# Kernel tuning notes

Hardware: AMD Instinct MI355X
Metric: run time of the kernel (lower is better)

## Reference

```python
import jax, jax.numpy as jnp
import numpy as np

B, S, E, D_ENT, D_HID, D_ATT = 8, 512, 32, 256, 512, 200

def setup_inputs() -> dict:
    key = jax.random.key(0)
    k1, k2, k3, k4, k5 = jax.random.split(key, 5)
    return {
        "cxt": jax.random.normal(k1, (B, S, D_HID), dtype=jnp.float32),
        "ent": jax.random.normal(k2, (B, S, E, D_ENT), dtype=jnp.float32),
        "We": jax.random.normal(k3, (D_ENT, D_ATT), dtype=jnp.float32) * 0.05,
        "Wh": jax.random.normal(k4, (D_HID, D_ATT), dtype=jnp.float32) * 0.05,
        "Ws": jax.random.normal(k5, (D_ATT, 1), dtype=jnp.float32) * 0.05,
    }

def reference(cxt, ent, We, Wh, Ws):
    # cxt: [B,S,H], ent: [B,S,E,D]
    cmean = jnp.mean(cxt, axis=1)                      # [B,H]  (mean context)
    h_att = cmean @ Wh                                 # [B,A]  shared across (s,e)
    e_att = jnp.einsum('bsed,da->bsea', ent, We)       # [B,S,E,A]
    M = jnp.tanh(h_att[:, None, None, :] + e_att)      # [B,S,E,A]
    S_logits = jnp.einsum('bsea,ao->bse', M, Ws)       # [B,S,E] (Ws has out dim 1)
    S_att = jax.nn.softmax(S_logits, axis=-1)          # softmax over entities
    # diag-matmul + sum in the original == weighted sum over entities
    ent_att = jnp.einsum('bse,bsed->bsd', S_att, ent)  # [B,S,D]
    return ent_att
```

## Files before the change

### kernel.cpp

```cpp
#include <hip/hip_runtime.h>
#include <math.h>

#define NB 8
#define NS 512
#define NE 32
#define DE 256
#define DH 512
#define DA 200
#define DAP 224
#define NJ 7

typedef __bf16 bf16x8 __attribute__((ext_vector_type(8)));
typedef float f32x16 __attribute__((ext_vector_type(16)));

__device__ __forceinline__ float tanh_fast(float x) {
    float e = __expf(x + x);
    return fmaf(-2.f, __builtin_amdgcn_rcpf(e + 1.f), 1.f);
}

__global__ __launch_bounds__(256) void cmean_partial(const float* __restrict__ cxt,
                                                     float* __restrict__ psum) {
    const int g = blockIdx.x;
    const int b = g >> 6, c = g & 63;
    const int t = threadIdx.x;
    const float* base = cxt + ((size_t)b * NS + c * 8) * DH;
    float s0 = 0.f, s1 = 0.f;
    #pragma unroll
    for (int s = 0; s < 8; ++s) {
        s0 += base[s * DH + t];
        s1 += base[s * DH + t + 256];
    }
    psum[(size_t)g * DH + t]       = s0;
    psum[(size_t)g * DH + t + 256] = s1;
}

__global__ __launch_bounds__(256) void hatt_from_psum(const float* __restrict__ psum,
                                                      const float* __restrict__ Wh,
                                                      float* __restrict__ hattw) {
    const int b = blockIdx.x;
    const int t = threadIdx.x;
    __shared__ float cm[DH];
    float s0 = 0.f, s1 = 0.f;
    for (int c = 0; c < 64; ++c) {
        s0 += psum[((size_t)b * 64 + c) * DH + t];
        s1 += psum[((size_t)b * 64 + c) * DH + t + 256];
    }
    cm[t]       = s0 * (1.f / NS);
    cm[t + 256] = s1 * (1.f / NS);
    __syncthreads();
    if (t < DAP) {
        float acc = 0.f;
        if (t < DA)
            for (int h = 0; h < DH; ++h)
                acc = fmaf(cm[h], Wh[h * DA + t], acc);
        hattw[b * DAP + t] = acc;
    }
}

__global__ __launch_bounds__(64) void wef_build(const float* __restrict__ We,
                                                __bf16* __restrict__ wef) {
    const int f = blockIdx.x;
    const int l = threadIdx.x;
    const int nj = f >> 4, kk = f & 15;
    const int n = nj * 32 + (l & 31);
    bf16x8 v;
    #pragma unroll
    for (int e = 0; e < 8; ++e) {
        int K = kk * 16 + ((l >> 5) << 2) + (e & 3) + 8 * (e >> 2);
        v[e] = (__bf16)((n < DA) ? We[K * DA + n] : 0.f);
    }
    reinterpret_cast<bf16x8*>(wef)[f * 64 + l] = v;
}

__global__ __launch_bounds__(1024) void entatt_main(const float* __restrict__ ent,
                                                    const __bf16* __restrict__ wef,
                                                    const float* __restrict__ hattw,
                                                    const float* __restrict__ Ws,
                                                    float* __restrict__ out) {
    const int t    = threadIdx.x;
    const int lane = t & 63;
    const int wid  = t >> 6;
    const int g    = blockIdx.x;
    const int bs   = g * 16 + wid;
    const int b    = g >> 5;

    __shared__ __bf16 wef_lds[NJ * 16 * 512];
    __shared__ float  hatt_lds[DAP];
    __shared__ float  ws_lds[DAP];
    __shared__ float  lg_lds[16][NE];

    {
        const float4* s4 = reinterpret_cast<const float4*>(wef);
        float4* d4 = reinterpret_cast<float4*>(wef_lds);
        #pragma unroll
        for (int i = 0; i < NJ; ++i) d4[t + i * 1024] = s4[t + i * 1024];
    }
    if (t < DAP) {
        hatt_lds[t] = hattw[b * DAP + t];
        ws_lds[t]   = (t < DA) ? Ws[t] : 0.f;
    }

    __syncthreads();

    const int m  = lane & 31;
    const int hi = lane >> 5;
    const float* eb = ent + (size_t)bs * (NE * DE);

    bf16x8 A[16];
    #pragma unroll
    for (int kk = 0; kk < 16; ++kk) {
        const float* p = eb + m * DE + kk * 16 + hi * 4;
        float4 u0 = *reinterpret_cast<const float4*>(p);
        float4 u1 = *reinterpret_cast<const float4*>(p + 8);
        bf16x8 v = { (__bf16)u0.x, (__bf16)u0.y, (__bf16)u0.z, (__bf16)u0.w,
                     (__bf16)u1.x, (__bf16)u1.y, (__bf16)u1.z, (__bf16)u1.w };
        A[kk] = v;
    }

    const bf16x8* w8 = reinterpret_cast<const bf16x8*>(wef_lds);

    float part[16];
    #pragma unroll
    for (int r = 0; r < 16; ++r) part[r] = 0.f;

    #pragma unroll 1
    for (int nj = 0; nj < NJ; ++nj) {
        f32x16 acc;
        #pragma unroll
        for (int r = 0; r < 16; ++r) acc[r] = 0.f;
        #pragma unroll
        for (int kk = 0; kk < 16; ++kk)
            acc = __builtin_amdgcn_mfma_f32_32x32x16_bf16(
                      A[kk], w8[(nj * 16 + kk) * 64 + lane], acc, 0, 0, 0);
        const float ha  = hatt_lds[nj * 32 + m];
        const float wsa = ws_lds[nj * 32 + m];
        #pragma unroll
        for (int r = 0; r < 16; ++r)
            part[r] = fmaf(tanh_fast(acc[r] + ha), wsa, part[r]);
    }

    #pragma unroll
    for (int r = 0; r < 16; ++r) {
        float v = part[r];
        v += __shfl_xor(v, 1);  v += __shfl_xor(v, 2);  v += __shfl_xor(v, 4);
        v += __shfl_xor(v, 8);  v += __shfl_xor(v, 16);
        part[r] = v;
    }
    if (m == 0) {
        #pragma unroll
        for (int r = 0; r < 16; ++r)
            lg_lds[wid][(r & 3) + 8 * (r >> 2) + 4 * hi] = part[r];
    }

    float mx = -1e30f;
    #pragma unroll
    for (int e = 0; e < NE; ++e) mx = fmaxf(mx, lg_lds[wid][e]);

    const float4* eb4 = reinterpret_cast<const float4*>(eb);
    float wsum = 0.f;
    float4 o = make_float4(0.f, 0.f, 0.f, 0.f);
    #pragma unroll
    for (int e = 0; e < NE; ++e) {
        float w = __expf(lg_lds[wid][e] - mx);
        wsum += w;
        float4 v = eb4[e * 64 + lane];
        o.x = fmaf(w, v.x, o.x); o.y = fmaf(w, v.y, o.y);
        o.z = fmaf(w, v.z, o.z); o.w = fmaf(w, v.w, o.w);
    }
    const float inv = __builtin_amdgcn_rcpf(wsum);
    float4 res = make_float4(o.x * inv, o.y * inv, o.z * inv, o.w * inv);
    reinterpret_cast<float4*>(out)[(size_t)bs * 64 + lane] = res;
}

extern "C" void kernel_launch(void* const* d_in, const int* in_sizes, int n_in,
                              void* d_out, int out_size, void* d_ws, size_t ws_size,
                              hipStream_t stream) {
    const float* cxt = (const float*)d_in[0];
    const float* ent = (const float*)d_in[1];
    const float* We  = (const float*)d_in[2];
    const float* Wh  = (const float*)d_in[3];
    const float* Ws  = (const float*)d_in[4];
    float* out = (float*)d_out;

    float*  psum  = (float*)d_ws;
    float*  hattw = psum + 512 * DH;
    __bf16* wef   = (__bf16*)(hattw + NB * DAP);

    hipLaunchKernelGGL(wef_build, dim3(NJ * 16), dim3(64), 0, stream, We, wef);
    hipLaunchKernelGGL(cmean_partial, dim3(512), dim3(256), 0, stream, cxt, psum);
    hipLaunchKernelGGL(hatt_from_psum, dim3(NB), dim3(256), 0, stream, psum, Wh, hattw);
    hipLaunchKernelGGL(entatt_main, dim3(256), dim3(1024), 0, stream,
                       ent, wef, hattw, Ws, out);
}
```

Measured before the change: 78.51 us.

## Process two (b,s) rows per wave with prefetch of second tile during compute

```diff
diff --git a/kernel.cpp b/kernel.cpp
--- a/kernel.cpp
+++ b/kernel.cpp
@@ -72,51 +72,16 @@
     reinterpret_cast<bf16x8*>(wef)[f * 64 + l] = v;
 }
 
-__global__ __launch_bounds__(1024) void entatt_main(const float* __restrict__ ent,
-                                                    const __bf16* __restrict__ wef,
-                                                    const float* __restrict__ hattw,
-                                                    const float* __restrict__ Ws,
-                                                    float* __restrict__ out) {
-    const int t    = threadIdx.x;
-    const int lane = t & 63;
-    const int wid  = t >> 6;
-    const int g    = blockIdx.x;
-    const int bs   = g * 16 + wid;
-    const int b    = g >> 5;
-
-    __shared__ __bf16 wef_lds[NJ * 16 * 512];
-    __shared__ float  hatt_lds[DAP];
-    __shared__ float  ws_lds[DAP];
-    __shared__ float  lg_lds[16][NE];
-
-    {
-        const float4* s4 = reinterpret_cast<const float4*>(wef);
-        float4* d4 = reinterpret_cast<float4*>(wef_lds);
-        #pragma unroll
-        for (int i = 0; i < NJ; ++i) d4[t + i * 1024] = s4[t + i * 1024];
-    }
-    if (t < DAP) {
-        hatt_lds[t] = hattw[b * DAP + t];
-        ws_lds[t]   = (t < DA) ? Ws[t] : 0.f;
-    }
-
-    __syncthreads();
-
+__device__ __forceinline__ void compute_tile(const bf16x8 (&A)[16],
+                                             const __bf16* __restrict__ wef_lds,
+                                             const float* __restrict__ hatt_lds,
+                                             const float* __restrict__ ws_lds,
+                                             const float* __restrict__ eb,
+                                             float* __restrict__ out,
+                                             float* __restrict__ lg_scratch,
+                                             int bs, int lane) {
     const int m  = lane & 31;
     const int hi = lane >> 5;
-    const float* eb = ent + (size_t)bs * (NE * DE);
-
-    bf16x8 A[16];
-    #pragma unroll
-    for (int kk = 0; kk < 16; ++kk) {
-        const float* p = eb + m * DE + kk * 16 + hi * 4;
-        float4 u0 = *reinterpret_cast<const float4*>(p);
-        float4 u1 = *reinterpret_cast<const float4*>(p + 8);
-        bf16x8 v = { (__bf16)u0.x, (__bf16)u0.y, (__bf16)u0.z, (__bf16)u0.w,
-                     (__bf16)u1.x, (__bf16)u1.y, (__bf16)u1.z, (__bf16)u1.w };
-        A[kk] = v;
-    }
-
     const bf16x8* w8 = reinterpret_cast<const bf16x8*>(wef_lds);
 
     float part[16];
@@ -149,19 +114,19 @@
     if (m == 0) {
         #pragma unroll
         for (int r = 0; r < 16; ++r)
-            lg_lds[wid][(r & 3) + 8 * (r >> 2) + 4 * hi] = part[r];
+            lg_scratch[(r & 3) + 8 * (r >> 2) + 4 * hi] = part[r];
     }
 
     float mx = -1e30f;
     #pragma unroll
-    for (int e = 0; e < NE; ++e) mx = fmaxf(mx, lg_lds[wid][e]);
+    for (int e = 0; e < NE; ++e) mx = fmaxf(mx, lg_scratch[e]);
 
     const float4* eb4 = reinterpret_cast<const float4*>(eb);
     float wsum = 0.f;
     float4 o = make_float4(0.f, 0.f, 0.f, 0.f);
     #pragma unroll
     for (int e = 0; e < NE; ++e) {
-        float w = __expf(lg_lds[wid][e] - mx);
+        float w = __expf(lg_scratch[e] - mx);
         wsum += w;
         float4 v = eb4[e * 64 + lane];
         o.x = fmaf(w, v.x, o.x); o.y = fmaf(w, v.y, o.y);
@@ -170,6 +135,83 @@
     const float inv = __builtin_amdgcn_rcpf(wsum);
     float4 res = make_float4(o.x * inv, o.y * inv, o.z * inv, o.w * inv);
     reinterpret_cast<float4*>(out)[(size_t)bs * 64 + lane] = res;
+}
+
+__global__ __launch_bounds__(512) void entatt_main(const float* __restrict__ ent,
+                                                   const __bf16* __restrict__ wef,
+                                                   const float* __restrict__ hattw,
+                                                   const float* __restrict__ Ws,
+                                                   float* __restrict__ out) {
+    const int t    = threadIdx.x;
+    const int lane = t & 63;
+    const int wid  = t >> 6;
+    const int g    = blockIdx.x;
+    const int bs0  = g * 16 + wid * 2;
+    const int b    = g >> 5;
+
+    __shared__ __bf16 wef_lds[NJ * 16 * 512];
+    __shared__ float  hatt_lds[DAP];
+    __shared__ float  ws_lds[DAP];
+    __shared__ float  lg_lds[8][NE];
+
+    {
+        const float4* s4 = reinterpret_cast<const float4*>(wef);
+        float4* d4 = reinterpret_cast<float4*>(wef_lds);
+        #pragma unroll
+        for (int i = 0; i < 14; ++i) d4[t + i * 512] = s4[t + i * 512];
+    }
+    if (t < DAP) {
+        hatt_lds[t] = hattw[b * DAP + t];
+        ws_lds[t]   = (t < DA) ? Ws[t] : 0.f;
+    }
+
+    __syncthreads();
+
+    const int m  = lane & 31;
+    const int hi = lane >> 5;
+    const float* e0 = ent + (size_t)bs0 * (NE * DE);
+    const float* e1 = e0 + NE * DE;
+
+    float4 u[32];
+    #pragma unroll
+    for (int kk = 0; kk < 16; ++kk) {
+        const float* p = e0 + m * DE + kk * 16 + hi * 4;
+        u[2 * kk]     = *reinterpret_cast<const float4*>(p);
+        u[2 * kk + 1] = *reinterpret_cast<const float4*>(p + 8);
+    }
+    __builtin_amdgcn_sched_barrier(0);
+
+    bf16x8 A0[16];
+    #pragma unroll
+    for (int kk = 0; kk < 16; ++kk) {
+        float4 a = u[2 * kk], c = u[2 * kk + 1];
+        bf16x8 v = { (__bf16)a.x, (__bf16)a.y, (__bf16)a.z, (__bf16)a.w,
+                     (__bf16)c.x, (__bf16)c.y, (__bf16)c.z, (__bf16)c.w };
+        A0[kk] = v;
+    }
+
+    float4 v1[32];
+    #pragma unroll
+    for (int kk = 0; kk < 16; ++kk) {
+        const float* p = e1 + m * DE + kk * 16 + hi * 4;
+        v1[2 * kk]     = *reinterpret_cast<const float4*>(p);
+        v1[2 * kk + 1] = *reinterpret_cast<const float4*>(p + 8);
+    }
+    __builtin_amdgcn_sched_barrier(0);
+
+    compute_tile(A0, wef_lds, hatt_lds, ws_lds, e0, out, lg_lds[wid], bs0, lane);
+
+    bf16x8 A1[16];
+    #pragma unroll
+    for (int kk = 0; kk < 16; ++kk) {
+        float4 a = v1[2 * kk], c = v1[2 * kk + 1];
+        bf16x8 v = { (__bf16)a.x, (__bf16)a.y, (__bf16)a.z, (__bf16)a.w,
+                     (__bf16)c.x, (__bf16)c.y, (__bf16)c.z, (__bf16)c.w };
+        A1[kk] = v;
+    }
+    __builtin_amdgcn_sched_barrier(0);
+
+    compute_tile(A1, wef_lds, hatt_lds, ws_lds, e1, out, lg_lds[wid], bs0 + 1, lane);
 }
 
 extern "C" void kernel_launch(void* const* d_in, const int* in_sizes, int n_in,
@@ -189,6 +231,6 @@
     hipLaunchKernelGGL(wef_build, dim3(NJ * 16), dim3(64), 0, stream, We, wef);
     hipLaunchKernelGGL(cmean_partial, dim3(512), dim3(256), 0, stream, cxt, psum);
     hipLaunchKernelGGL(hatt_from_psum, dim3(NB), dim3(256), 0, stream, psum, Wh, hattw);
-    hipLaunchKernelGGL(entatt_main, dim3(256), dim3(1024), 0, stream,
+    hipLaunchKernelGGL(entatt_main, dim3(256), dim3(512), 0, stream,
                        ent, wef, hattw, Ws, out);
 }
```

After: 80.70 us. +2.8%, slower.

## Stage entity tiles through double-buffered LDS with register-resident weight fragments

Applied to the files above, without the earlier changes.

```diff
diff --git a/kernel.cpp b/kernel.cpp
--- a/kernel.cpp
+++ b/kernel.cpp
@@ -72,104 +72,131 @@
     reinterpret_cast<bf16x8*>(wef)[f * 64 + l] = v;
 }
 
-__global__ __launch_bounds__(1024) void entatt_main(const float* __restrict__ ent,
-                                                    const __bf16* __restrict__ wef,
-                                                    const float* __restrict__ hattw,
-                                                    const float* __restrict__ Ws,
-                                                    float* __restrict__ out) {
+__global__ __launch_bounds__(512) void entatt_main(const float* __restrict__ ent,
+                                                   const __bf16* __restrict__ wef,
+                                                   const float* __restrict__ hattw,
+                                                   const float* __restrict__ Ws,
+                                                   float* __restrict__ out) {
     const int t    = threadIdx.x;
     const int lane = t & 63;
     const int wid  = t >> 6;
+    const int m    = lane & 31;
+    const int hi   = lane >> 5;
     const int g    = blockIdx.x;
-    const int bs   = g * 16 + wid;
     const int b    = g >> 5;
 
-    __shared__ __bf16 wef_lds[NJ * 16 * 512];
-    __shared__ float  hatt_lds[DAP];
-    __shared__ float  ws_lds[DAP];
-    __shared__ float  lg_lds[16][NE];
+    __shared__ float buf[2][16384];
+    __shared__ float partials[2][NJ][NE];
+
+    bf16x8 B[16];
+    float ha = 0.f, wsa = 0.f;
+    if (wid < NJ) {
+        const bf16x8* wef8 = reinterpret_cast<const bf16x8*>(wef);
+        #pragma unroll
+        for (int kk = 0; kk < 16; ++kk) B[kk] = wef8[(wid * 16 + kk) * 64 + lane];
+        const int a = wid * 32 + m;
+        ha  = hattw[b * DAP + a];
+        wsa = (a < DA) ? Ws[a] : 0.f;
+    }
+
+    float4 u[8];
 
     {
-        const float4* s4 = reinterpret_cast<const float4*>(wef);
-        float4* d4 = reinterpret_cast<float4*>(wef_lds);
+        const size_t base = (size_t)(g * 16) * 8192;
         #pragma unroll
-        for (int i = 0; i < NJ; ++i) d4[t + i * 1024] = s4[t + i * 1024];
-    }
-    if (t < DAP) {
-        hatt_lds[t] = hattw[b * DAP + t];
-        ws_lds[t]   = (t < DA) ? Ws[t] : 0.f;
-    }
-
+        for (int j = 0; j < 8; ++j) {
+            const int Rj = wid * 8 + j;
+            const int mR = Rj & 31;
+            const float* src = ent + base + (size_t)(Rj >> 5) * 8192
+                             + mR * 256 + ((lane ^ mR) << 2);
+            u[j] = *reinterpret_cast<const float4*>(src);
+        }
+        __builtin_amdgcn_sched_barrier(0);
+        float4* d4 = reinterpret_cast<float4*>(buf[0]);
+        #pragma unroll
+        for (int j = 0; j < 8; ++j) d4[(wid * 8 + j) * 64 + lane] = u[j];
+    }
     __syncthreads();
 
-    const int m  = lane & 31;
-    const int hi = lane >> 5;
-    const float* eb = ent + (size_t)bs * (NE * DE);
-
-    bf16x8 A[16];
-    #pragma unroll
-    for (int kk = 0; kk < 16; ++kk) {
-        const float* p = eb + m * DE + kk * 16 + hi * 4;
-        float4 u0 = *reinterpret_cast<const float4*>(p);
-        float4 u1 = *reinterpret_cast<const float4*>(p + 8);
-        bf16x8 v = { (__bf16)u0.x, (__bf16)u0.y, (__bf16)u0.z, (__bf16)u0.w,
-                     (__bf16)u1.x, (__bf16)u1.y, (__bf16)u1.z, (__bf16)u1.w };
-        A[kk] = v;
-    }
-
-    const bf16x8* w8 = reinterpret_cast<const bf16x8*>(wef_lds);
-
-    float part[16];
-    #pragma unroll
-    for (int r = 0; r < 16; ++r) part[r] = 0.f;
-
     #pragma unroll 1
-    for (int nj = 0; nj < NJ; ++nj) {
-        f32x16 acc;
-        #pragma unroll
-        for (int r = 0; r < 16; ++r) acc[r] = 0.f;
-        #pragma unroll
-        for (int kk = 0; kk < 16; ++kk)
-            acc = __builtin_amdgcn_mfma_f32_32x32x16_bf16(
-                      A[kk], w8[(nj * 16 + kk) * 64 + lane], acc, 0, 0, 0);
-        const float ha  = hatt_lds[nj * 32 + m];
-        const float wsa = ws_lds[nj * 32 + m];
-        #pragma unroll
-        for (int r = 0; r < 16; ++r)
-            part[r] = fmaf(tanh_fast(acc[r] + ha), wsa, part[r]);
-    }
-
-    #pragma unroll
-    for (int r = 0; r < 16; ++r) {
-        float v = part[r];
-        v += __shfl_xor(v, 1);  v += __shfl_xor(v, 2);  v += __shfl_xor(v, 4);
-        v += __shfl_xor(v, 8);  v += __shfl_xor(v, 16);
-        part[r] = v;
-    }
-    if (m == 0) {
-        #pragma unroll
-        for (int r = 0; r < 16; ++r)
-            lg_lds[wid][(r & 3) + 8 * (r >> 2) + 4 * hi] = part[r];
-    }
-
-    float mx = -1e30f;
-    #pragma unroll
-    for (int e = 0; e < NE; ++e) mx = fmaxf(mx, lg_lds[wid][e]);
-
-    const float4* eb4 = reinterpret_cast<const float4*>(eb);
-    float wsum = 0.f;
-    float4 o = make_float4(0.f, 0.f, 0.f, 0.f);
-    #pragma unroll
-    for (int e = 0; e < NE; ++e) {
-        float w = __expf(lg_lds[wid][e] - mx);
-        wsum += w;
-        float4 v = eb4[e * 64 + lane];
-        o.x = fmaf(w, v.x, o.x); o.y = fmaf(w, v.y, o.y);
-        o.z = fmaf(w, v.z, o.z); o.w = fmaf(w, v.w, o.w);
-    }
-    const float inv = __builtin_amdgcn_rcpf(wsum);
-    float4 res = make_float4(o.x * inv, o.y * inv, o.z * inv, o.w * inv);
-    reinterpret_cast<float4*>(out)[(size_t)bs * 64 + lane] = res;
+    for (int r = 0; r < 8; ++r) {
+        const int cur = r & 1;
+
+        if (r < 7) {
+            const size_t base = (size_t)(g * 16 + (r + 1) * 2) * 8192;
+            #pragma unroll
+            for (int j = 0; j < 8; ++j) {
+                const int Rj = wid * 8 + j;
+                const int mR = Rj & 31;
+                const float* src = ent + base + (size_t)(Rj >> 5) * 8192
+                                 + mR * 256 + ((lane ^ mR) << 2);
+                u[j] = *reinterpret_cast<const float4*>(src);
+            }
+            __builtin_amdgcn_sched_barrier(0);
+        }
+
+        if (wid < NJ) {
+            #pragma unroll
+            for (int tau = 0; tau < 2; ++tau) {
+                const float4* bf4 = reinterpret_cast<const float4*>(&buf[cur][tau * 8192]);
+                f32x16 acc;
+                #pragma unroll
+                for (int q = 0; q < 16; ++q) acc[q] = 0.f;
+                #pragma unroll
+                for (int kk = 0; kk < 16; ++kk) {
+                    const int k0 = kk * 4 + hi;
+                    float4 p0 = bf4[m * 64 + (k0 ^ m)];
+                    float4 p1 = bf4[m * 64 + ((k0 + 2) ^ m)];
+                    bf16x8 fr = { (__bf16)p0.x, (__bf16)p0.y, (__bf16)p0.z, (__bf16)p0.w,
+                                  (__bf16)p1.x, (__bf16)p1.y, (__bf16)p1.z, (__bf16)p1.w };
+                    acc = __builtin_amdgcn_mfma_f32_32x32x16_bf16(fr, B[kk], acc, 0, 0, 0);
+                }
+                #pragma unroll
+                for (int q = 0; q < 16; ++q) {
+                    float v = tanh_fast(acc[q] + ha) * wsa;
+                    v += __shfl_xor(v, 1);  v += __shfl_xor(v, 2);  v += __shfl_xor(v, 4);
+                    v += __shfl_xor(v, 8);  v += __shfl_xor(v, 16);
+                    if (m == 0)
+                        partials[tau][wid][(q & 3) + 8 * (q >> 2) + 4 * hi] = v;
+                }
+            }
+        }
+        __syncthreads();
+
+        {
+            const int tau = wid >> 2;
+            const int q4  = wid & 3;
+            const int e0  = lane & 31;
+            float lg = 0.f;
+            #pragma unroll
+            for (int w = 0; w < NJ; ++w) lg += partials[tau][w][e0];
+            float mx = lg;
+            mx = fmaxf(mx, __shfl_xor(mx, 1));  mx = fmaxf(mx, __shfl_xor(mx, 2));
+            mx = fmaxf(mx, __shfl_xor(mx, 4));  mx = fmaxf(mx, __shfl_xor(mx, 8));
+            mx = fmaxf(mx, __shfl_xor(mx, 16));
+            float ex = __expf(lg - mx);
+            float sm = ex;
+            sm += __shfl_xor(sm, 1);  sm += __shfl_xor(sm, 2);  sm += __shfl_xor(sm, 4);
+            sm += __shfl_xor(sm, 8);  sm += __shfl_xor(sm, 16);
+            const float wv = ex * __builtin_amdgcn_rcpf(sm);
+            const float* bt = &buf[cur][tau * 8192];
+            const int d = q4 * 64 + lane;
+            float o = 0.f;
+            #pragma unroll
+            for (int e = 0; e < NE; ++e) {
+                float we = __shfl(wv, e);
+                o = fmaf(we, bt[e * 256 + (d ^ (e << 2))], o);
+            }
+            out[(size_t)(g * 16 + r * 2 + tau) * 256 + d] = o;
+        }
+
+        if (r < 7) {
+            float4* d4 = reinterpret_cast<float4*>(buf[cur ^ 1]);
+            #pragma unroll
+            for (int j = 0; j < 8; ++j) d4[(wid * 8 + j) * 64 + lane] = u[j];
+        }
+        __syncthreads();
+    }
 }
 
 extern "C" void kernel_launch(void* const* d_in, const int* in_sizes, int n_in,
@@ -189,6 +216,6 @@
     hipLaunchKernelGGL(wef_build, dim3(NJ * 16), dim3(64), 0, stream, We, wef);
     hipLaunchKernelGGL(cmean_partial, dim3(512), dim3(256), 0, stream, cxt, psum);
     hipLaunchKernelGGL(hatt_from_psum, dim3(NB), dim3(256), 0, stream, psum, Wh, hattw);
-    hipLaunchKernelGGL(entatt_main, dim3(256), dim3(1024), 0, stream,
+    hipLaunchKernelGGL(entatt_main, dim3(256), dim3(512), 0, stream,
                        ent, wef, hattw, Ws, out);
 }
```

Result: slower. 151.3 us (+92.8%).

## Pre-pack entity tensor into bf16 MFMA fragment layout in a separate pass

Applied to the files above, without the earlier changes.

```diff
diff --git a/kernel.cpp b/kernel.cpp
--- a/kernel.cpp
+++ b/kernel.cpp
@@ -72,11 +72,39 @@
     reinterpret_cast<bf16x8*>(wef)[f * 64 + l] = v;
 }
 
-__global__ __launch_bounds__(1024) void entatt_main(const float* __restrict__ ent,
-                                                    const __bf16* __restrict__ wef,
-                                                    const float* __restrict__ hattw,
-                                                    const float* __restrict__ Ws,
-                                                    float* __restrict__ out) {
+__global__ __launch_bounds__(256) void entf_build(const float* __restrict__ ent,
+                                                  __bf16* __restrict__ entf) {
+    const int bs = blockIdx.x;
+    const int t  = threadIdx.x;
+    __shared__ float L[32 * 260];
+    const float4* s4 = reinterpret_cast<const float4*>(ent + (size_t)bs * 8192);
+    #pragma unroll
+    for (int i = 0; i < 8; ++i) {
+        float4 v = s4[t + i * 256];
+        int f4 = t + i * 256;
+        int m = f4 >> 6, c4 = f4 & 63;
+        *reinterpret_cast<float4*>(&L[m * 260 + c4 * 4]) = v;
+    }
+    __syncthreads();
+    bf16x8* dst = reinterpret_cast<bf16x8*>(entf) + (size_t)bs * 1024;
+    #pragma unroll
+    for (int q = 0; q < 4; ++q) {
+        int idx  = q * 256 + t;
+        int kk   = idx >> 6, lane = idx & 63;
+        int m    = lane & 31, hi = lane >> 5;
+        const float* p = &L[m * 260 + kk * 16 + hi * 4];
+        bf16x8 v = { (__bf16)p[0], (__bf16)p[1], (__bf16)p[2],  (__bf16)p[3],
+                     (__bf16)p[8], (__bf16)p[9], (__bf16)p[10], (__bf16)p[11] };
+        dst[idx] = v;
+    }
+}
+
+__global__ __launch_bounds__(1024) void entatt_main_frag(const float* __restrict__ ent,
+                                                         const __bf16* __restrict__ entf,
+                                                         const __bf16* __restrict__ wef,
+                                                         const float* __restrict__ hattw,
+                                                         const float* __restrict__ Ws,
+                                                         float* __restrict__ out) {
     const int t    = threadIdx.x;
     const int lane = t & 63;
     const int wid  = t >> 6;
@@ -100,6 +128,98 @@
         ws_lds[t]   = (t < DA) ? Ws[t] : 0.f;
     }
 
+    __syncthreads();
+
+    const int m  = lane & 31;
+    const int hi = lane >> 5;
+
+    const bf16x8* ef8 = reinterpret_cast<const bf16x8*>(entf) + (size_t)bs * 1024 + lane;
+    bf16x8 A[16];
+    #pragma unroll
+    for (int kk = 0; kk < 16; ++kk) A[kk] = ef8[kk * 64];
+
+    const bf16x8* w8 = reinterpret_cast<const bf16x8*>(wef_lds);
+
+    float part[16];
+    #pragma unroll
+    for (int r = 0; r < 16; ++r) part[r] = 0.f;
+
+    #pragma unroll 1
+    for (int nj = 0; nj < NJ; ++nj) {
+        f32x16 acc;
+        #pragma unroll
+        for (int r = 0; r < 16; ++r) acc[r] = 0.f;
+        #pragma unroll
+        for (int kk = 0; kk < 16; ++kk)
+            acc = __builtin_amdgcn_mfma_f32_32x32x16_bf16(
+                      A[kk], w8[(nj * 16 + kk) * 64 + lane], acc, 0, 0, 0);
+        const float ha  = hatt_lds[nj * 32 + m];
+        const float wsa = ws_lds[nj * 32 + m];
+        #pragma unroll
+        for (int r = 0; r < 16; ++r)
+            part[r] = fmaf(tanh_fast(acc[r] + ha), wsa, part[r]);
+    }
+
+    #pragma unroll
+    for (int r = 0; r < 16; ++r) {
+        float v = part[r];
+        v += __shfl_xor(v, 1);  v += __shfl_xor(v, 2);  v += __shfl_xor(v, 4);
+        v += __shfl_xor(v, 8);  v += __shfl_xor(v, 16);
+        part[r] = v;
+    }
+    if (m == 0) {
+        #pragma unroll
+        for (int r = 0; r < 16; ++r)
+            lg_lds[wid][(r & 3) + 8 * (r >> 2) + 4 * hi] = part[r];
+    }
+
+    float mx = -1e30f;
+    #pragma unroll
+    for (int e = 0; e < NE; ++e) mx = fmaxf(mx, lg_lds[wid][e]);
+
+    const float4* eb4 = reinterpret_cast<const float4*>(ent + (size_t)bs * (NE * DE));
+    float wsum = 0.f;
+    float4 o = make_float4(0.f, 0.f, 0.f, 0.f);
+    #pragma unroll
+    for (int e = 0; e < NE; ++e) {
+        float w = __expf(lg_lds[wid][e] - mx);
+        wsum += w;
+        float4 v = eb4[e * 64 + lane];
+        o.x = fmaf(w, v.x, o.x); o.y = fmaf(w, v.y, o.y);
+        o.z = fmaf(w, v.z, o.z); o.w = fmaf(w, v.w, o.w);
+    }
+    const float inv = __builtin_amdgcn_rcpf(wsum);
+    float4 res = make_float4(o.x * inv, o.y * inv, o.z * inv, o.w * inv);
+    reinterpret_cast<float4*>(out)[(size_t)bs * 64 + lane] = res;
+}
+
+__global__ __launch_bounds__(1024) void entatt_main_direct(const float* __restrict__ ent,
+                                                           const __bf16* __restrict__ wef,
+                                                           const float* __restrict__ hattw,
+                                                           const float* __restrict__ Ws,
+                                                           float* __restrict__ out) {
+    const int t    = threadIdx.x;
+    const int lane = t & 63;
+    const int wid  = t >> 6;
+    const int g    = blockIdx.x;
+    const int bs   = g * 16 + wid;
+    const int b    = g >> 5;
+
+    __shared__ __bf16 wef_lds[NJ * 16 * 512];
+    __shared__ float  hatt_lds[DAP];
+    __shared__ float  ws_lds[DAP];
+    __shared__ float  lg_lds[16][NE];
+
+    {
+        const float4* s4 = reinterpret_cast<const float4*>(wef);
+        float4* d4 = reinterpret_cast<float4*>(wef_lds);
+        #pragma unroll
+        for (int i = 0; i < NJ; ++i) d4[t + i * 1024] = s4[t + i * 1024];
+    }
+    if (t < DAP) {
+        hatt_lds[t] = hattw[b * DAP + t];
+        ws_lds[t]   = (t < DA) ? Ws[t] : 0.f;
+    }
     __syncthreads();
 
     const int m  = lane & 31;
@@ -118,7 +238,6 @@
     }
 
     const bf16x8* w8 = reinterpret_cast<const bf16x8*>(wef_lds);
-
     float part[16];
     #pragma unroll
     for (int r = 0; r < 16; ++r) part[r] = 0.f;
@@ -182,13 +301,24 @@
     const float* Ws  = (const float*)d_in[4];
     float* out = (float*)d_out;
 
-    float*  psum  = (float*)d_ws;
-    float*  hattw = psum + 512 * DH;
-    __bf16* wef   = (__bf16*)(hattw + NB * DAP);
+    char* ws = (char*)d_ws;
+    float*  psum  = (float*)ws;
+    float*  hattw = (float*)(ws + 512 * DH * 4);
+    __bf16* wef   = (__bf16*)(ws + 512 * DH * 4 + NB * DAP * 4);
+    const size_t entf_off = 512 * DH * 4 + NB * DAP * 4 + (size_t)NJ * 16 * 512 * 2;
+    __bf16* entf  = (__bf16*)(ws + entf_off);
+    const size_t need = entf_off + (size_t)NB * NS * NE * DE * 2;
 
     hipLaunchKernelGGL(wef_build, dim3(NJ * 16), dim3(64), 0, stream, We, wef);
     hipLaunchKernelGGL(cmean_partial, dim3(512), dim3(256), 0, stream, cxt, psum);
     hipLaunchKernelGGL(hatt_from_psum, dim3(NB), dim3(256), 0, stream, psum, Wh, hattw);
-    hipLaunchKernelGGL(entatt_main, dim3(256), dim3(1024), 0, stream,
-                       ent, wef, hattw, Ws, out);
-}
+
+    if (ws_size >= need) {
+        hipLaunchKernelGGL(entf_build, dim3(NB * NS), dim3(256), 0, stream, ent, entf);
+        hipLaunchKernelGGL(entatt_main_frag, dim3(256), dim3(1024), 0, stream,
+                           ent, entf, wef, hattw, Ws, out);
+    } else {
+        hipLaunchKernelGGL(entatt_main_direct, dim3(256), dim3(1024), 0, stream,
+                           ent, wef, hattw, Ws, out);
+    }
+}
```

Result: slower. 98.53 us (+25.5%).
